# Performance work log

Hardware: AMD Instinct MI355X
Metric: run time of the kernel (lower is better)

Reference implementation:

```python
import jax, jax.numpy as jnp
import numpy as np

B, N, D, H = 2, 2048, 1024, 16
DH = D // H


def setup_inputs() -> dict:
    key = jax.random.key(0)
    ks = jax.random.split(key, 5)
    s = 0.02
    return {
        "x": jax.random.normal(ks[0], (B, N, D), dtype=jnp.float32),
        "Wq": jax.random.normal(ks[1], (D, D), dtype=jnp.float32) * s,
        "Wk": jax.random.normal(ks[2], (D, D), dtype=jnp.float32) * s,
        "Wv": jax.random.normal(ks[3], (D, D), dtype=jnp.float32) * s,
        "Wo": jax.random.normal(ks[4], (D, D), dtype=jnp.float32) * s,
        "bo": jnp.zeros((D,), dtype=jnp.float32),
    }


def reference(x, Wq, Wk, Wv, Wo, bo):
    b, n, d = x.shape
    # linear projections (torch Linear: y = x @ W.T), split into heads -> [b,h,n,dh]
    def proj(W):
        return jnp.einsum('bnd,ed->bne', x, W).reshape(b, n, H, DH).transpose(0, 2, 1, 3)
    q, k, v = proj(Wq), proj(Wk), proj(Wv)
    scores = jnp.einsum('bhqd,bhkd->bhqk', q, k)  # [b,h,n,n]
    causal = jnp.triu(jnp.ones((n, n), dtype=bool), k=1)
    scores = jnp.where(causal, -jnp.inf, scores)
    # NOTE: module scales by 1/sqrt(num_key_tokens), not 1/sqrt(d_head)
    w = jax.nn.softmax(scores / jnp.sqrt(jnp.float32(n)), axis=-1)
    ctx = jnp.einsum('bhqk,bhkd->bhqd', w, v)
    ctx = ctx.transpose(0, 2, 1, 3).reshape(b, n, d)
    return jnp.einsum('bnd,ed->bne', ctx, Wo) + bo
```

## Files before the change

kernel.cpp:

```cpp
#include <hip/hip_runtime.h>
#include <hip/hip_bf16.h>

typedef __attribute__((ext_vector_type(8))) short bf16x8;
typedef __attribute__((ext_vector_type(4))) float f32x4;
typedef __attribute__((ext_vector_type(16))) float f32x16;
typedef unsigned short u16;

__device__ __forceinline__ u16 f2bf(float f) {
  union { float f; unsigned int u; } v; v.f = f;
  return (u16)((v.u + 0x7fffu + ((v.u >> 16) & 1u)) >> 16);
}
__device__ __forceinline__ unsigned int pack_bf2(float f0, float f1) {
  union { float f; unsigned int u; } a, b; a.f = f0; b.f = f1;
  return __builtin_amdgcn_perm(b.u + 0x8000u, a.u + 0x8000u, 0x07060302u);
}

#define GLOAD_LDS16(g, l) __builtin_amdgcn_global_load_lds( \
    (const __attribute__((address_space(1))) void*)(g),     \
    (__attribute__((address_space(3))) void*)(l), 16, 0, 0)

__global__ __launch_bounds__(256) void conv_all(const float* __restrict__ x,
                                                const float* __restrict__ wq, const float* __restrict__ wk,
                                                const float* __restrict__ wv, const float* __restrict__ wo,
                                                u16* __restrict__ xb, u16* __restrict__ qo, u16* __restrict__ ko,
                                                u16* __restrict__ vo, u16* __restrict__ oo) {
  int y = blockIdx.y;
  const float* src; u16* dst;
  if (y < 4) { src = x + (size_t)y * 1048576; dst = xb + (size_t)y * 1048576; }
  else if (y == 4) { src = wq; dst = qo; }
  else if (y == 5) { src = wk; dst = ko; }
  else if (y == 6) { src = wv; dst = vo; }
  else { src = wo; dst = oo; }
  int i = (blockIdx.x * 256 + threadIdx.x) * 4;
  float4 v = *(const float4*)(src + i);
  ushort4 o;
  o.x = f2bf(v.x); o.y = f2bf(v.y); o.z = f2bf(v.z); o.w = f2bf(v.w);
  *(ushort4*)(dst + i) = o;
}

template <bool SW>
__device__ __forceinline__ void gemm_main(const u16* __restrict__ A, const u16* __restrict__ W,
                                          u16* As, u16* Bs, int m0, int n0, int K,
                                          f32x4 acc[4][4]) {
  int tid = threadIdx.x, wave = tid >> 6, lane = tid & 63;
  int lane15 = lane & 15, quad = lane >> 4;
  int wm = (wave >> 1) * 64, wn = (wave & 1) * 64;
  for (int k0 = 0; k0 < K; k0 += 64) {
    __syncthreads();
#pragma unroll
    for (int i = 0; i < 4; i++) {
      int rbase = wave * 32 + i * 8;
      int rloc = rbase + (lane >> 3);
      int ca = ((lane & 7) ^ (rloc & 7)) * 8;
      GLOAD_LDS16(A + (size_t)(m0 + rloc) * K + k0 + ca, As + rbase * 64);
      GLOAD_LDS16(W + (size_t)(n0 + rloc) * K + k0 + ca, Bs + rbase * 64);
    }
    __syncthreads();
#pragma unroll
    for (int kc = 0; kc < 2; kc++) {
      bf16x8 a[4], b[4];
#pragma unroll
      for (int mi = 0; mi < 4; mi++) {
        int m = wm + mi * 16 + lane15;
        a[mi] = *(const bf16x8*)(As + m * 64 + (((kc * 4 + quad) ^ (m & 7)) * 8));
      }
#pragma unroll
      for (int ni = 0; ni < 4; ni++) {
        int n = wn + ni * 16 + lane15;
        b[ni] = *(const bf16x8*)(Bs + n * 64 + (((kc * 4 + quad) ^ (n & 7)) * 8));
      }
#pragma unroll
      for (int mi = 0; mi < 4; mi++)
#pragma unroll
        for (int ni = 0; ni < 4; ni++)
          acc[mi][ni] = SW ? __builtin_amdgcn_mfma_f32_16x16x32_bf16(b[ni], a[mi], acc[mi][ni], 0, 0, 0)
                           : __builtin_amdgcn_mfma_f32_16x16x32_bf16(a[mi], b[ni], acc[mi][ni], 0, 0, 0);
    }
  }
}

__global__ __launch_bounds__(256, 3) void gemm_qkv(const u16* __restrict__ xb,
                                                   const u16* __restrict__ wq, const u16* __restrict__ wk,
                                                   const u16* __restrict__ wv,
                                                   u16* __restrict__ Qb, u16* __restrict__ Kb,
                                                   u16* __restrict__ Vtg) {
  __shared__ __align__(16) u16 As[128 * 64];
  __shared__ __align__(16) u16 Bs[128 * 64];
  const int K = 1024;
  int z = blockIdx.z;
  const u16* W = (z == 0) ? wq : (z == 1) ? wk : wv;
  int m0 = blockIdx.x * 128, n0 = blockIdx.y * 128;
  f32x4 acc[4][4];
#pragma unroll
  for (int i = 0; i < 4; i++)
#pragma unroll
    for (int j = 0; j < 4; j++) acc[i][j] = (f32x4){0.f, 0.f, 0.f, 0.f};

  int tid = threadIdx.x, wave = tid >> 6, lane = tid & 63;
  int lane15 = lane & 15, quad = lane >> 4;
  int wm = (wave >> 1) * 64, wn = (wave & 1) * 64;
  const float kQs = 0.022097086912079608f * 1.4426950408889634f;

  if (z < 2) {
    gemm_main<true>(xb, W, As, Bs, m0, n0, K, acc);
    u16* Out = z ? Kb : Qb;
    float sc = z ? 1.0f : kQs;
#pragma unroll
    for (int mi = 0; mi < 4; mi++)
#pragma unroll
      for (int ni = 0; ni < 4; ni++) {
        int token = m0 + wm + mi * 16 + lane15;
        int fb = n0 + wn + ni * 16 + quad * 4;
        ushort4 o;
        o.x = f2bf(acc[mi][ni][0] * sc); o.y = f2bf(acc[mi][ni][1] * sc);
        o.z = f2bf(acc[mi][ni][2] * sc); o.w = f2bf(acc[mi][ni][3] * sc);
        *(ushort4*)&Out[(size_t)token * 1024 + fb] = o;
      }
  } else {
    gemm_main<false>(xb, W, As, Bs, m0, n0, K, acc);
#pragma unroll
    for (int mi = 0; mi < 4; mi++)
#pragma unroll
      for (int ni = 0; ni < 4; ni++) {
        int row = m0 + wm + mi * 16 + quad * 4;
        int col = n0 + wn + ni * 16 + lane15;
        int bb = row >> 11, nn = row & 2047;
        ushort4 o;
        o.x = f2bf(acc[mi][ni][0]); o.y = f2bf(acc[mi][ni][1]);
        o.z = f2bf(acc[mi][ni][2]); o.w = f2bf(acc[mi][ni][3]);
        *(ushort4*)&Vtg[(size_t)(bb * 1024 + col) * 2048 + nn] = o;
      }
  }
}

__global__ __launch_bounds__(256, 2) void gemm_out(const u16* __restrict__ A, const u16* __restrict__ W,
                                                   float* __restrict__ Of, const float* __restrict__ bias) {
  __shared__ __align__(16) u16 As[128 * 64];
  __shared__ __align__(16) u16 Bs[64 * 64];
  const int K = 1024;
  int m0 = blockIdx.x * 128, n0 = blockIdx.y * 64;
  int tid = threadIdx.x, wave = tid >> 6, lane = tid & 63;
  int lane15 = lane & 15, quad = lane >> 4;
  int wm = (wave >> 1) * 64, wn = (wave & 1) * 32;
  f32x4 acc[4][2];
#pragma unroll
  for (int i = 0; i < 4; i++)
#pragma unroll
    for (int j = 0; j < 2; j++) acc[i][j] = (f32x4){0.f, 0.f, 0.f, 0.f};
  for (int k0 = 0; k0 < K; k0 += 64) {
    __syncthreads();
#pragma unroll
    for (int i = 0; i < 4; i++) {
      int rbase = wave * 32 + i * 8;
      int rloc = rbase + (lane >> 3);
      int ca = ((lane & 7) ^ (rloc & 7)) * 8;
      GLOAD_LDS16(A + (size_t)(m0 + rloc) * K + k0 + ca, As + rbase * 64);
    }
#pragma unroll
    for (int i = 0; i < 2; i++) {
      int rbase = wave * 16 + i * 8;
      int rloc = rbase + (lane >> 3);
      int ca = ((lane & 7) ^ (rloc & 7)) * 8;
      GLOAD_LDS16(W + (size_t)(n0 + rloc) * K + k0 + ca, Bs + rbase * 64);
    }
    __syncthreads();
#pragma unroll
    for (int kc = 0; kc < 2; kc++) {
      bf16x8 a[4], b[2];
#pragma unroll
      for (int mi = 0; mi < 4; mi++) {
        int m = wm + mi * 16 + lane15;
        a[mi] = *(const bf16x8*)(As + m * 64 + (((kc * 4 + quad) ^ (m & 7)) * 8));
      }
#pragma unroll
      for (int ni = 0; ni < 2; ni++) {
        int n = wn + ni * 16 + lane15;
        b[ni] = *(const bf16x8*)(Bs + n * 64 + (((kc * 4 + quad) ^ (n & 7)) * 8));
      }
#pragma unroll
      for (int mi = 0; mi < 4; mi++)
#pragma unroll
        for (int ni = 0; ni < 2; ni++)
          acc[mi][ni] = __builtin_amdgcn_mfma_f32_16x16x32_bf16(b[ni], a[mi], acc[mi][ni], 0, 0, 0);
    }
  }
#pragma unroll
  for (int mi = 0; mi < 4; mi++)
#pragma unroll
    for (int ni = 0; ni < 2; ni++) {
      int token = m0 + wm + mi * 16 + lane15;
      int fb = n0 + wn + ni * 16 + quad * 4;
      float4 bb = *(const float4*)&bias[fb];
      float4 o;
      o.x = acc[mi][ni][0] + bb.x; o.y = acc[mi][ni][1] + bb.y;
      o.z = acc[mi][ni][2] + bb.z; o.w = acc[mi][ni][3] + bb.w;
      *(float4*)&Of[(size_t)token * 1024 + fb] = o;
    }
}

__global__ __launch_bounds__(256, 2) void attn6(const u16* __restrict__ Q, const u16* __restrict__ Kg,
                                                const u16* __restrict__ Vtg, u16* __restrict__ ctx) {
  __shared__ __align__(16) u16 SH[24576];
  int tid = threadIdx.x, wave = tid >> 6, lane = tid & 63;
  int l31 = lane & 31, hf = lane >> 5;
  int qt = wave & 1, kvh = wave >> 1;

  int g = blockIdx.x, bh = blockIdx.y;
  int b = bh >> 4, h = bh & 15;
  int tA = g, tB = 31 - g;
  int qbase[2] = {g * 64, (31 - g) * 64};

  bf16x8 qb[2][4];
#pragma unroll
  for (int st = 0; st < 2; st++)
#pragma unroll
    for (int s = 0; s < 4; s++)
      qb[st][s] = *(const bf16x8*)&Q[(size_t)(b * 2048 + qbase[st] + qt * 32 + l31) * 1024 +
                                     h * 64 + s * 16 + hf * 8];

  f32x16 oacc[2][2];
#pragma unroll
  for (int st = 0; st < 2; st++)
#pragma unroll
    for (int dt = 0; dt < 2; dt++)
#pragma unroll
      for (int r = 0; r < 16; r++) oacc[st][dt][r] = 0.f;
  float lsum[2] = {0.f, 0.f};

  auto stage = [&](int t, int d) {
    int tb = t * 64;
    u16* Kd = SH + d * 4096;
    u16* Vd = SH + 8192 + d * 4096;
#pragma unroll
    for (int i = 0; i < 2; i++) {
      int rbase = wave * 16 + i * 8;
      int rk = rbase + (lane >> 3);
      int ca = ((lane & 7) ^ (rk & 7)) * 8;
      GLOAD_LDS16(&Kg[(size_t)(b * 2048 + tb + rk) * 1024 + h * 64 + ca], Kd + rbase * 64);
      GLOAD_LDS16(&Vtg[(size_t)(b * 1024 + h * 64 + rk) * 2048 + tb + ca], Vd + rbase * 64);
    }
  };

  u16* Ps = SH + 16384;
  int psw = (l31 & 3) << 1;

  stage(0, 0);
  for (int t = 0; t <= tB; ++t) {
    __syncthreads();
    if (t < tB) stage(t + 1, (t + 1) & 1);
    int d = t & 1;
    const u16* Kd = SH + d * 4096;
    const u16* Vd = SH + 8192 + d * 4096;

    int krow = kvh * 32 + l31;
    const u16* kp = Kd + krow * 64;
    bf16x8 kf[4];
#pragma unroll
    for (int s = 0; s < 4; s++)
      kf[s] = *(const bf16x8*)(kp + (((2 * s + hf) ^ (krow & 7)) * 8));
    bf16x8 vf[2][2];
#pragma unroll
    for (int dt = 0; dt < 2; dt++) {
      int vrow = dt * 32 + l31;
#pragma unroll
      for (int c = 0; c < 2; c++)
        vf[dt][c] = *(const bf16x8*)(Vd + vrow * 64 + (((4 * kvh + 2 * c + hf) ^ (vrow & 7)) * 8));
    }

#pragma unroll
    for (int st = 0; st < 2; st++) {
      bool active = st ? true : (t <= tA);
      bool diag = st ? (t == tB) : (t == tA);
      if (!active) continue;
      if (diag && kvh > qt) continue;

      f32x16 sv;
#pragma unroll
      for (int r = 0; r < 16; r++) sv[r] = 0.f;
#pragma unroll
      for (int s = 0; s < 4; s++)
        sv = __builtin_amdgcn_mfma_f32_32x32x16_bf16(kf[s], qb[st][s], sv, 0, 0, 0);

      if (diag && kvh == qt) {
#pragma unroll
        for (int r = 0; r < 16; r++) {
          int kvloc = (r & 3) + 8 * (r >> 2) + 4 * hf;
          if (kvloc > l31) sv[r] = -10000.0f;
        }
      }
#pragma unroll
      for (int r = 0; r < 16; r++) {
        float p = __builtin_amdgcn_exp2f(sv[r]);
        sv[r] = p; lsum[st] += p;
      }
      u16* pr = Ps + (wave * 2 + st) * 1024 + l31 * 32;
#pragma unroll
      for (int gr = 0; gr < 4; gr++) {
        unsigned int lo = pack_bf2(sv[4 * gr + 0], sv[4 * gr + 1]);
        unsigned int hi = pack_bf2(sv[4 * gr + 2], sv[4 * gr + 3]);
        int u = (2 * gr + hf) ^ psw;
        *(uint2*)(pr + u * 4) = (uint2){lo, hi};
      }
#pragma unroll
      for (int c = 0; c < 2; c++) {
        int u0 = (4 * c + 2 * hf) ^ psw;
        bf16x8 pf = *(const bf16x8*)(pr + u0 * 4);
#pragma unroll
        for (int dt = 0; dt < 2; dt++)
          oacc[st][dt] = __builtin_amdgcn_mfma_f32_32x32x16_bf16(vf[dt][c], pf, oacc[st][dt], 0, 0, 0);
      }
    }
  }

  lsum[0] += __shfl_xor(lsum[0], 32);
  lsum[1] += __shfl_xor(lsum[1], 32);
  float* MG = (float*)SH;
  float* LS = (float*)(SH + 16384);
  __syncthreads();
  if (kvh == 1) {
#pragma unroll
    for (int st = 0; st < 2; st++) {
#pragma unroll
      for (int dt = 0; dt < 2; dt++) {
        float* p = MG + (((qt * 2 + st) * 2 + dt) * 64 + lane) * 16;
#pragma unroll
        for (int q4 = 0; q4 < 4; q4++)
          *(f32x4*)(p + q4 * 4) = (f32x4){oacc[st][dt][4 * q4], oacc[st][dt][4 * q4 + 1],
                                          oacc[st][dt][4 * q4 + 2], oacc[st][dt][4 * q4 + 3]};
      }
      LS[(qt * 2 + st) * 32 + l31] = lsum[st];
    }
  }
  __syncthreads();
  if (kvh == 0) {
#pragma unroll
    for (int st = 0; st < 2; st++) {
      float inv = 1.0f / (lsum[st] + LS[(qt * 2 + st) * 32 + l31]);
      int token = qbase[st] + qt * 32 + l31;
      size_t off = (size_t)(b * 2048 + token) * 1024 + h * 64;
#pragma unroll
      for (int dt = 0; dt < 2; dt++) {
        const float* p = MG + (((qt * 2 + st) * 2 + dt) * 64 + lane) * 16;
#pragma unroll
        for (int gr = 0; gr < 4; gr++) {
          f32x4 m = *(const f32x4*)(p + gr * 4);
          ushort4 o;
          o.x = f2bf((oacc[st][dt][4 * gr + 0] + m[0]) * inv);
          o.y = f2bf((oacc[st][dt][4 * gr + 1] + m[1]) * inv);
          o.z = f2bf((oacc[st][dt][4 * gr + 2] + m[2]) * inv);
          o.w = f2bf((oacc[st][dt][4 * gr + 3] + m[3]) * inv);
          *(ushort4*)&ctx[off + dt * 32 + 8 * gr + 4 * hf] = o;
        }
      }
    }
  }
}

extern "C" void kernel_launch(void* const* d_in, const int* in_sizes, int n_in,
                              void* d_out, int out_size, void* d_ws, size_t ws_size,
                              hipStream_t stream) {
  const float* x  = (const float*)d_in[0];
  const float* Wq = (const float*)d_in[1];
  const float* Wk = (const float*)d_in[2];
  const float* Wv = (const float*)d_in[3];
  const float* Wo = (const float*)d_in[4];
  const float* bo = (const float*)d_in[5];
  float* out = (float*)d_out;
  char* ws = (char*)d_ws;
  const size_t MB = 1024 * 1024;
  u16* xb   = (u16*)(ws);
  u16* wqb  = (u16*)(ws +  8 * MB);
  u16* wkb  = (u16*)(ws + 10 * MB);
  u16* wvb  = (u16*)(ws + 12 * MB);
  u16* wob  = (u16*)(ws + 14 * MB);
  u16* Qb   = (u16*)(ws + 16 * MB);
  u16* Kb   = (u16*)(ws + 24 * MB);
  u16* Vtg  = (u16*)(ws + 32 * MB);
  u16* ctxb = (u16*)(ws + 40 * MB);

  conv_all<<<dim3(1024, 8), 256, 0, stream>>>(x, Wq, Wk, Wv, Wo, xb, wqb, wkb, wvb, wob);
  gemm_qkv<<<dim3(32, 8, 3), 256, 0, stream>>>(xb, wqb, wkb, wvb, Qb, Kb, Vtg);
  attn6<<<dim3(16, 32), 256, 0, stream>>>(Qb, Kb, Vtg, ctxb);
  gemm_out<<<dim3(32, 16), 256, 0, stream>>>(ctxb, wob, out, bo);
}
```

Before: 173.2 us.

## Split paired query tiles into separate blocks and pass P via cross-lane shuffles

Each attention block previously handled two query tiles (g and 31-g) to balance causal work. Now each block handles one 64-row query tile, giving twice as many blocks, ordered so that the longest tiles launch first. The P matrix is now rearranged into the MFMA B-operand layout with cross-lane shuffles instead of a round trip through LDS. LDS drops to 32KB and the occupancy hint rises to 4, which lifts parallelism and occupancy. The cost is that K/V tiles are reloaded for each query tile, and the per-block work is now unbalanced.

```diff
diff --git a/kernel.cpp b/kernel.cpp
--- a/kernel.cpp
+++ b/kernel.cpp
@@ -5,12 +5,13 @@
 typedef __attribute__((ext_vector_type(4))) float f32x4;
 typedef __attribute__((ext_vector_type(16))) float f32x16;
 typedef unsigned short u16;
+typedef unsigned int u32;
 
 __device__ __forceinline__ u16 f2bf(float f) {
   union { float f; unsigned int u; } v; v.f = f;
   return (u16)((v.u + 0x7fffu + ((v.u >> 16) & 1u)) >> 16);
 }
-__device__ __forceinline__ unsigned int pack_bf2(float f0, float f1) {
+__device__ __forceinline__ u32 pack_bf2(float f0, float f1) {
   union { float f; unsigned int u; } a, b; a.f = f0; b.f = f1;
   return __builtin_amdgcn_perm(b.u + 0x8000u, a.u + 0x8000u, 0x07060302u);
 }
@@ -198,34 +199,30 @@
     }
 }
 
-__global__ __launch_bounds__(256, 2) void attn6(const u16* __restrict__ Q, const u16* __restrict__ Kg,
+__global__ __launch_bounds__(256, 4) void attn7(const u16* __restrict__ Q, const u16* __restrict__ Kg,
                                                 const u16* __restrict__ Vtg, u16* __restrict__ ctx) {
-  __shared__ __align__(16) u16 SH[24576];
+  __shared__ __align__(16) u16 SH[16384];
   int tid = threadIdx.x, wave = tid >> 6, lane = tid & 63;
   int l31 = lane & 31, hf = lane >> 5;
   int qt = wave & 1, kvh = wave >> 1;
 
-  int g = blockIdx.x, bh = blockIdx.y;
+  int bh = blockIdx.x, by = blockIdx.y;
+  int sidx = (by < 16) ? (31 - by) : (by - 16);
   int b = bh >> 4, h = bh & 15;
-  int tA = g, tB = 31 - g;
-  int qbase[2] = {g * 64, (31 - g) * 64};
-
-  bf16x8 qb[2][4];
-#pragma unroll
-  for (int st = 0; st < 2; st++)
-#pragma unroll
-    for (int s = 0; s < 4; s++)
-      qb[st][s] = *(const bf16x8*)&Q[(size_t)(b * 2048 + qbase[st] + qt * 32 + l31) * 1024 +
-                                     h * 64 + s * 16 + hf * 8];
-
-  f32x16 oacc[2][2];
-#pragma unroll
-  for (int st = 0; st < 2; st++)
-#pragma unroll
-    for (int dt = 0; dt < 2; dt++)
-#pragma unroll
-      for (int r = 0; r < 16; r++) oacc[st][dt][r] = 0.f;
-  float lsum[2] = {0.f, 0.f};
+  int qbase = sidx * 64;
+
+  bf16x8 qb[4];
+#pragma unroll
+  for (int s = 0; s < 4; s++)
+    qb[s] = *(const bf16x8*)&Q[(size_t)(b * 2048 + qbase + qt * 32 + l31) * 1024 +
+                               h * 64 + s * 16 + hf * 8];
+
+  f32x16 oacc[2];
+#pragma unroll
+  for (int dt = 0; dt < 2; dt++)
+#pragma unroll
+    for (int r = 0; r < 16; r++) oacc[dt][r] = 0.f;
+  float lsum = 0.f;
 
   auto stage = [&](int t, int d) {
     int tb = t * 64;
@@ -241,116 +238,102 @@
     }
   };
 
-  u16* Ps = SH + 16384;
-  int psw = (l31 & 3) << 1;
-
   stage(0, 0);
-  for (int t = 0; t <= tB; ++t) {
-    __syncthreads();
-    if (t < tB) stage(t + 1, (t + 1) & 1);
+  for (int t = 0; t <= sidx; ++t) {
+    __syncthreads();
+    if (t < sidx) stage(t + 1, (t + 1) & 1);
     int d = t & 1;
     const u16* Kd = SH + d * 4096;
     const u16* Vd = SH + 8192 + d * 4096;
 
+    bool diag = (t == sidx);
+    if (diag && kvh > qt) continue;
+
     int krow = kvh * 32 + l31;
     const u16* kp = Kd + krow * 64;
     bf16x8 kf[4];
 #pragma unroll
     for (int s = 0; s < 4; s++)
       kf[s] = *(const bf16x8*)(kp + (((2 * s + hf) ^ (krow & 7)) * 8));
-    bf16x8 vf[2][2];
-#pragma unroll
-    for (int dt = 0; dt < 2; dt++) {
-      int vrow = dt * 32 + l31;
-#pragma unroll
-      for (int c = 0; c < 2; c++)
-        vf[dt][c] = *(const bf16x8*)(Vd + vrow * 64 + (((4 * kvh + 2 * c + hf) ^ (vrow & 7)) * 8));
-    }
-
-#pragma unroll
-    for (int st = 0; st < 2; st++) {
-      bool active = st ? true : (t <= tA);
-      bool diag = st ? (t == tB) : (t == tA);
-      if (!active) continue;
-      if (diag && kvh > qt) continue;
-
-      f32x16 sv;
-#pragma unroll
-      for (int r = 0; r < 16; r++) sv[r] = 0.f;
-#pragma unroll
-      for (int s = 0; s < 4; s++)
-        sv = __builtin_amdgcn_mfma_f32_32x32x16_bf16(kf[s], qb[st][s], sv, 0, 0, 0);
-
-      if (diag && kvh == qt) {
-#pragma unroll
-        for (int r = 0; r < 16; r++) {
-          int kvloc = (r & 3) + 8 * (r >> 2) + 4 * hf;
-          if (kvloc > l31) sv[r] = -10000.0f;
-        }
-      }
+
+    f32x16 sv;
+#pragma unroll
+    for (int r = 0; r < 16; r++) sv[r] = 0.f;
+#pragma unroll
+    for (int s = 0; s < 4; s++)
+      sv = __builtin_amdgcn_mfma_f32_32x32x16_bf16(kf[s], qb[s], sv, 0, 0, 0);
+
+    if (diag && kvh == qt) {
 #pragma unroll
       for (int r = 0; r < 16; r++) {
-        float p = __builtin_amdgcn_exp2f(sv[r]);
-        sv[r] = p; lsum[st] += p;
-      }
-      u16* pr = Ps + (wave * 2 + st) * 1024 + l31 * 32;
-#pragma unroll
-      for (int gr = 0; gr < 4; gr++) {
-        unsigned int lo = pack_bf2(sv[4 * gr + 0], sv[4 * gr + 1]);
-        unsigned int hi = pack_bf2(sv[4 * gr + 2], sv[4 * gr + 3]);
-        int u = (2 * gr + hf) ^ psw;
-        *(uint2*)(pr + u * 4) = (uint2){lo, hi};
-      }
-#pragma unroll
-      for (int c = 0; c < 2; c++) {
-        int u0 = (4 * c + 2 * hf) ^ psw;
-        bf16x8 pf = *(const bf16x8*)(pr + u0 * 4);
-#pragma unroll
-        for (int dt = 0; dt < 2; dt++)
-          oacc[st][dt] = __builtin_amdgcn_mfma_f32_32x32x16_bf16(vf[dt][c], pf, oacc[st][dt], 0, 0, 0);
-      }
-    }
-  }
-
-  lsum[0] += __shfl_xor(lsum[0], 32);
-  lsum[1] += __shfl_xor(lsum[1], 32);
+        int kvloc = (r & 3) + 8 * (r >> 2) + 4 * hf;
+        if (kvloc > l31) sv[r] = -10000.0f;
+      }
+    }
+#pragma unroll
+    for (int r = 0; r < 16; r++) {
+      float p = __builtin_amdgcn_exp2f(sv[r]);
+      sv[r] = p; lsum += p;
+    }
+    u32 p0 = pack_bf2(sv[0], sv[1]),   p1 = pack_bf2(sv[2], sv[3]);
+    u32 p2 = pack_bf2(sv[4], sv[5]),   p3 = pack_bf2(sv[6], sv[7]);
+    u32 p4 = pack_bf2(sv[8], sv[9]),   p5 = pack_bf2(sv[10], sv[11]);
+    u32 p6 = pack_bf2(sv[12], sv[13]), p7 = pack_bf2(sv[14], sv[15]);
+    u32 x0 = __shfl_xor(hf ? p0 : p2, 32);
+    u32 x1 = __shfl_xor(hf ? p1 : p3, 32);
+    u32 x2 = __shfl_xor(hf ? p4 : p6, 32);
+    u32 x3 = __shfl_xor(hf ? p5 : p7, 32);
+    union U8 { u32 u[4]; bf16x8 v; };
+    U8 pf0, pf1;
+    pf0.u[0] = hf ? x0 : p0; pf0.u[1] = hf ? x1 : p1;
+    pf0.u[2] = hf ? p2 : x0; pf0.u[3] = hf ? p3 : x1;
+    pf1.u[0] = hf ? x2 : p4; pf1.u[1] = hf ? x3 : p5;
+    pf1.u[2] = hf ? p6 : x2; pf1.u[3] = hf ? p7 : x3;
+
+#pragma unroll
+    for (int c = 0; c < 2; c++) {
+      bf16x8 pf = c ? pf1.v : pf0.v;
+#pragma unroll
+      for (int dt = 0; dt < 2; dt++) {
+        int vrow = dt * 32 + l31;
+        bf16x8 va = *(const bf16x8*)(Vd + vrow * 64 + (((4 * kvh + 2 * c + hf) ^ (vrow & 7)) * 8));
+        oacc[dt] = __builtin_amdgcn_mfma_f32_32x32x16_bf16(va, pf, oacc[dt], 0, 0, 0);
+      }
+    }
+  }
+
+  lsum += __shfl_xor(lsum, 32);
   float* MG = (float*)SH;
-  float* LS = (float*)(SH + 16384);
+  float* LS = (float*)(SH + 8192);
   __syncthreads();
   if (kvh == 1) {
 #pragma unroll
-    for (int st = 0; st < 2; st++) {
-#pragma unroll
-      for (int dt = 0; dt < 2; dt++) {
-        float* p = MG + (((qt * 2 + st) * 2 + dt) * 64 + lane) * 16;
-#pragma unroll
-        for (int q4 = 0; q4 < 4; q4++)
-          *(f32x4*)(p + q4 * 4) = (f32x4){oacc[st][dt][4 * q4], oacc[st][dt][4 * q4 + 1],
-                                          oacc[st][dt][4 * q4 + 2], oacc[st][dt][4 * q4 + 3]};
-      }
-      LS[(qt * 2 + st) * 32 + l31] = lsum[st];
-    }
+    for (int dt = 0; dt < 2; dt++) {
+      float* p = MG + ((qt * 2 + dt) * 64 + lane) * 16;
+#pragma unroll
+      for (int gr = 0; gr < 4; gr++)
+        *(f32x4*)(p + gr * 4) = (f32x4){oacc[dt][4 * gr], oacc[dt][4 * gr + 1],
+                                        oacc[dt][4 * gr + 2], oacc[dt][4 * gr + 3]};
+    }
+    LS[qt * 32 + l31] = lsum;
   }
   __syncthreads();
   if (kvh == 0) {
-#pragma unroll
-    for (int st = 0; st < 2; st++) {
-      float inv = 1.0f / (lsum[st] + LS[(qt * 2 + st) * 32 + l31]);
-      int token = qbase[st] + qt * 32 + l31;
-      size_t off = (size_t)(b * 2048 + token) * 1024 + h * 64;
-#pragma unroll
-      for (int dt = 0; dt < 2; dt++) {
-        const float* p = MG + (((qt * 2 + st) * 2 + dt) * 64 + lane) * 16;
-#pragma unroll
-        for (int gr = 0; gr < 4; gr++) {
-          f32x4 m = *(const f32x4*)(p + gr * 4);
-          ushort4 o;
-          o.x = f2bf((oacc[st][dt][4 * gr + 0] + m[0]) * inv);
-          o.y = f2bf((oacc[st][dt][4 * gr + 1] + m[1]) * inv);
-          o.z = f2bf((oacc[st][dt][4 * gr + 2] + m[2]) * inv);
-          o.w = f2bf((oacc[st][dt][4 * gr + 3] + m[3]) * inv);
-          *(ushort4*)&ctx[off + dt * 32 + 8 * gr + 4 * hf] = o;
-        }
+    float inv = 1.0f / (lsum + LS[qt * 32 + l31]);
+    int token = qbase + qt * 32 + l31;
+    size_t off = (size_t)(b * 2048 + token) * 1024 + h * 64;
+#pragma unroll
+    for (int dt = 0; dt < 2; dt++) {
+      const float* p = MG + ((qt * 2 + dt) * 64 + lane) * 16;
+#pragma unroll
+      for (int gr = 0; gr < 4; gr++) {
+        f32x4 m = *(const f32x4*)(p + gr * 4);
+        ushort4 o;
+        o.x = f2bf((oacc[dt][4 * gr + 0] + m[0]) * inv);
+        o.y = f2bf((oacc[dt][4 * gr + 1] + m[1]) * inv);
+        o.z = f2bf((oacc[dt][4 * gr + 2] + m[2]) * inv);
+        o.w = f2bf((oacc[dt][4 * gr + 3] + m[3]) * inv);
+        *(ushort4*)&ctx[off + dt * 32 + 8 * gr + 4 * hf] = o;
       }
     }
   }
@@ -380,6 +363,6 @@
 
   conv_all<<<dim3(1024, 8), 256, 0, stream>>>(x, Wq, Wk, Wv, Wo, xb, wqb, wkb, wvb, wob);
   gemm_qkv<<<dim3(32, 8, 3), 256, 0, stream>>>(xb, wqb, wkb, wvb, Qb, Kb, Vtg);
-  attn6<<<dim3(16, 32), 256, 0, stream>>>(Qb, Kb, Vtg, ctxb);
+  attn7<<<dim3(32, 32), 256, 0, stream>>>(Qb, Kb, Vtg, ctxb);
   gemm_out<<<dim3(32, 16), 256, 0, stream>>>(ctxb, wob, out, bo);
 }
```

Result: faster. 165.8 us (-4.2%).
